# Optimization experiments

Measured on AMD Instinct MI355X. Metric: run time of the kernel, lower is better.

## Reference

```python
import jax, jax.numpy as jnp
import numpy as np

REG = 10.0       # Sinkhorn entropic regularization (module default)
ALPHA = 1e-3     # residual blend coefficient (module default)
N_ITER = 200     # fixed Sinkhorn iterations (POT default numItermax=1000 w/ early stop)


def _sinkhorn(cost):
    """Standard (non-log) Sinkhorn as in POT's ot.sinkhorn. cost: (n, m)."""
    n, m = cost.shape
    a = jnp.full((n,), 1.0 / n, cost.dtype)
    b = jnp.full((m,), 1.0 / m, cost.dtype)
    K = jnp.exp(-cost / REG)                     # (n, m)
    u0 = jnp.full((n,), 1.0 / n, cost.dtype)
    v0 = jnp.full((m,), 1.0 / m, cost.dtype)

    def step(carry, _):
        u, v = carry
        v = b / (K.T @ u)
        u = a / (K @ v)
        return (u, v), None

    (u, v), _ = jax.lax.scan(step, (u0, v0), None, length=N_ITER)
    return (u[:, None] * K) * v[None, :]         # transport plan (n, m)


def setup_inputs() -> dict:
    key = jax.random.key(0)
    k1, k2 = jax.random.split(key)
    sc = jax.random.normal(k1, (4096, 256), dtype=jnp.float32)
    h_spot = jax.random.normal(k2, (4, 256, 48, 48), dtype=jnp.float32)
    return {"sc": sc, "h_spot": h_spot}


def reference(sc, h_spot):
    B, C, H, W = h_spot.shape
    sc_sub = sc[:, :C]                                  # (n_cells, C)
    Y = h_spot.reshape(B, C, H * W).transpose(0, 2, 1)  # (B, HW, C)

    # torch version detaches (numpy round-trip) before the OT solve
    X = jax.lax.stop_gradient(sc_sub)
    Y_sg = jax.lax.stop_gradient(Y)

    # squared Euclidean cost: ot.dist(X, Y, 'euclidean')**2
    x2 = jnp.sum(X * X, axis=-1)                        # (n_cells,)
    y2 = jnp.sum(Y_sg * Y_sg, axis=-1)                  # (B, HW)
    cost = x2[None, :, None] + y2[:, None, :] - 2.0 * jnp.einsum('nc,bmc->bnm', X, Y_sg)
    cost = jnp.maximum(cost, 0.0)                       # (B, n_cells, HW)

    P = jax.vmap(_sinkhorn)(cost)                       # (B, n_cells, HW)
    X_space = jnp.einsum('bnm,nc->bmc', P, X)           # (B, HW, C), detached in torch

    # mean over batch of per-batch MSE == overall mean (equal sizes)
    L_ot = jnp.mean((Y - X_space) ** 2)

    ot_feat = X_space.transpose(0, 2, 1).reshape(B, C, H, W)
    h_spot_aligned = h_spot + ALPHA * ot_feat
    return h_spot_aligned, L_ot, ot_feat
```

## Files before the change

### kernel.cpp

```cpp
#include <hip/hip_runtime.h>
#include <hip/hip_fp16.h>

#define NN 4096
#define NM 2304
#define NC 256
#define OUT_ELEMS 2359296
#define MAX_IT 10

static constexpr float REG_INV = 0.1f;
static constexpr float A_VAL = 1.0f / 4096.0f;
static constexpr float B_VAL = 1.0f / 2304.0f;
static constexpr float ALPHA_C = 0.001f;
static constexpr float EPS_CONV = 1e-4f;
static constexpr float S_Q = 6144.0f;

typedef __attribute__((ext_vector_type(8))) short bf16x8;
typedef __attribute__((ext_vector_type(4))) float f32x4;
typedef __attribute__((ext_vector_type(2))) float f32x2;

__device__ __forceinline__ float bf2f(unsigned short h) {
  return __uint_as_float(((unsigned int)h) << 16);
}
__device__ __forceinline__ unsigned short f2bf(float f) {
  unsigned int u = __float_as_uint(f);
  unsigned int r = (u + 0x7FFFu + ((u >> 16) & 1u)) >> 16;
  return (unsigned short)r;
}
__device__ __forceinline__ unsigned char f2e5(float x) {
  unsigned short h = __half_as_ushort(__float2half_rn(x));
  return (unsigned char)((h + 0x7Fu + ((h >> 8) & 1u)) >> 8);
}
__device__ __forceinline__ float e52f(unsigned int hs) {
  return __half2float(__ushort_as_half((unsigned short)hs));
}
__device__ __forceinline__ void dec4(unsigned int q, float4& o) {
#if __has_builtin(__builtin_amdgcn_cvt_pk_f32_bf8)
  f32x2 lo = __builtin_amdgcn_cvt_pk_f32_bf8((int)q, false);
  f32x2 hi = __builtin_amdgcn_cvt_pk_f32_bf8((int)q, true);
  o.x = lo[0]; o.y = lo[1]; o.z = hi[0]; o.w = hi[1];
#else
  o.x = e52f((q << 8) & 0xFF00u);
  o.y = e52f(q & 0xFF00u);
  o.z = e52f((q >> 8) & 0xFF00u);
  o.w = e52f((q >> 16) & 0xFF00u);
#endif
}
__device__ __forceinline__ float waveSum(float s) {
#pragma unroll
  for (int off = 32; off > 0; off >>= 1) s += __shfl_xor(s, off);
  return s;
}

__global__ __launch_bounds__(256) void x2_kernel(const float* __restrict__ X,
                                                 float* __restrict__ x2) {
  int wid = threadIdx.x >> 6, lane = threadIdx.x & 63;
  int row = blockIdx.x * 4 + wid;
  float4 v = *(const float4*)(X + (size_t)row * NC + lane * 4);
  float s = v.x * v.x + v.y * v.y + v.z * v.z + v.w * v.w;
  s = waveSum(s);
  if (lane == 0) x2[row] = s;
}

__global__ __launch_bounds__(256) void y2_kernel(const float* __restrict__ H,
                                                 float* __restrict__ y2) {
  const int b = blockIdx.y;
  const int m0 = blockIdx.x * 32;
  const int t = threadIdx.x;
  const int ml = t & 31, cg = t >> 5;
  const float* p = H + ((size_t)b * NC + cg) * NM + m0 + ml;
  float s = 0.f;
#pragma unroll 8
  for (int i = 0; i < 32; ++i) {
    float v = p[(size_t)i * 8 * NM];
    s += v * v;
  }
  __shared__ float red[8][33];
  red[cg][ml] = s;
  __syncthreads();
  if (t < 32) {
    float tot = 0.f;
#pragma unroll
    for (int g = 0; g < 8; ++g) tot += red[g][t];
    y2[b * NM + m0 + t] = tot;
  }
}

__global__ __launch_bounds__(256) void prep_xbf(const float* __restrict__ X,
                                                unsigned short* __restrict__ Xbf) {
  size_t i = blockIdx.x * 256 + threadIdx.x;
  float4 xv = *(const float4*)(X + i * 4);
  ushort4 o = {f2bf(xv.x), f2bf(xv.y), f2bf(xv.z), f2bf(xv.w)};
  *(ushort4*)(Xbf + i * 4) = o;
}

__global__ __launch_bounds__(256) void prep_ht(const float* __restrict__ H,
                                               unsigned short* __restrict__ HT) {
  __shared__ unsigned short tile[32][34];
  const int b = blockIdx.z;
  const int mt = blockIdx.x * 32, ct = blockIdx.y * 32;
  const int t = threadIdx.x;
#pragma unroll
  for (int p = 0; p < 4; ++p) {
    int c = ct + p * 8 + (t >> 5);
    tile[t & 31][p * 8 + (t >> 5)] = f2bf(H[((size_t)b * NC + c) * NM + mt + (t & 31)]);
  }
  __syncthreads();
#pragma unroll
  for (int p = 0; p < 4; ++p) {
    int mloc = p * 8 + (t >> 5);
    HT[((size_t)b * NM + mt + mloc) * NC + ct + (t & 31)] = tile[mloc][t & 31];
  }
}

__global__ __launch_bounds__(256) void umax_kernel(const float* __restrict__ uF,
                                                   float* __restrict__ umax) {
  const int b = blockIdx.x, t = threadIdx.x, l = t & 63, wv = t >> 6;
  float mx = 0.f;
  for (int i = t; i < NN; i += 256) mx = fmaxf(mx, uF[b * NN + i]);
#pragma unroll
  for (int off = 32; off > 0; off >>= 1) mx = fmaxf(mx, __shfl_xor(mx, off));
  __shared__ float wm[4];
  if (l == 0) wm[wv] = mx;
  __syncthreads();
  if (t == 0) umax[b] = fmaxf(fmaxf(wm[0], wm[1]), fmaxf(wm[2], wm[3]));
}

__global__ __launch_bounds__(256) void prep_xqu(const float* __restrict__ X,
                                                const float* __restrict__ uF,
                                                const float* __restrict__ umax,
                                                unsigned char* __restrict__ XquT) {
  __shared__ unsigned char tile[32][36];
  const int b = blockIdx.z;
  const int nt = blockIdx.x * 32, ct = blockIdx.y * 32;
  const int t = threadIdx.x;
  const float s = S_Q / umax[b];
#pragma unroll
  for (int p = 0; p < 4; ++p) {
    int nloc = p * 8 + (t >> 5);
    float uu = s * uF[b * NN + nt + nloc];
    tile[nloc][t & 31] = f2e5(uu * X[(size_t)(nt + nloc) * NC + ct + (t & 31)]);
  }
  __syncthreads();
  int cl = t >> 3, seg = t & 7;
  uchar4 o = {tile[seg * 4 + 0][cl], tile[seg * 4 + 1][cl],
              tile[seg * 4 + 2][cl], tile[seg * 4 + 3][cl]};
  *(uchar4*)(XquT + ((size_t)b * NC + ct + cl) * NN + nt + seg * 4) = o;
}

__global__ __launch_bounds__(256) void init_kernel(float* __restrict__ usum0,
                                                   float* __restrict__ u0,
                                                   int* __restrict__ nc) {
  int gid = blockIdx.x * 256 + threadIdx.x;
  usum0[gid] = 1.0f;
  u0[gid] = A_VAL;
  if (gid < 8) nc[gid] = 1;
}

__global__ __launch_bounds__(256) void cost_k_mfma(
    const unsigned short* __restrict__ Xbf, const unsigned short* __restrict__ HT,
    const float* __restrict__ x2, const float* __restrict__ y2,
    unsigned short* __restrict__ KT) {
  __shared__ __align__(16) unsigned short smem[128 * 88];
  const int b = blockIdx.z;
  const int n0 = blockIdx.x * 128, m0 = blockIdx.y * 128;
  const int t = threadIdx.x, l = t & 63, w = t >> 6;
  const int wn = (w >> 1) * 64, wm = (w & 1) * 64;
  const int fr = l & 15, fq = l >> 4;
  f32x4 zero = {0.f, 0.f, 0.f, 0.f};
  f32x4 acc[4][4];
#pragma unroll
  for (int i = 0; i < 4; ++i)
#pragma unroll
    for (int j = 0; j < 4; ++j) acc[i][j] = zero;

  for (int c0 = 0; c0 < NC; c0 += 32) {
#pragma unroll
    for (int i = 0; i < 2; ++i) {
      int idx = t + i * 256;
      int row = idx >> 2, ck = idx & 3;
      float4 av = *(const float4*)(Xbf + (size_t)(n0 + row) * NC + c0 + ck * 8);
      *(float4*)(&smem[row * 44 + ck * 8]) = av;
      float4 bv = *(const float4*)(HT + ((size_t)b * NM + m0 + row) * NC + c0 + ck * 8);
      *(float4*)(&smem[5632 + row * 44 + ck * 8]) = bv;
    }
    __syncthreads();
    bf16x8 a[4], bb[4];
#pragma unroll
    for (int f = 0; f < 4; ++f) {
      a[f] = *(const bf16x8*)(&smem[(wn + f * 16 + fr) * 44 + fq * 8]);
      bb[f] = *(const bf16x8*)(&smem[5632 + (wm + f * 16 + fr) * 44 + fq * 8]);
    }
#pragma unroll
    for (int i = 0; i < 4; ++i)
#pragma unroll
      for (int j = 0; j < 4; ++j)
        acc[i][j] = __builtin_amdgcn_mfma_f32_16x16x32_bf16(a[i], bb[j], acc[i][j], 0, 0, 0);
    __syncthreads();
  }
  float x2a[4][4];
#pragma unroll
  for (int fi = 0; fi < 4; ++fi) {
    float4 xv = *(const float4*)(x2 + n0 + wn + fi * 16 + fq * 4);
    x2a[fi][0] = xv.x; x2a[fi][1] = xv.y; x2a[fi][2] = xv.z; x2a[fi][3] = xv.w;
  }
  float y2a[4];
#pragma unroll
  for (int fj = 0; fj < 4; ++fj) y2a[fj] = y2[b * NM + m0 + wm + fj * 16 + fr];
  unsigned short kb[4][4][4];
#pragma unroll
  for (int fi = 0; fi < 4; ++fi)
#pragma unroll
    for (int fj = 0; fj < 4; ++fj)
#pragma unroll
      for (int r = 0; r < 4; ++r) {
        float cost = fmaxf(x2a[fi][r] + y2a[fj] - 2.0f * acc[fi][fj][r], 0.0f);
        kb[fi][fj][r] = f2bf(__expf(-cost * REG_INV));
      }
#pragma unroll
  for (int h = 0; h < 2; ++h) {
    __syncthreads();
    if ((w & 1) == h) {
#pragma unroll
      for (int fj = 0; fj < 4; ++fj) {
        int rr = fj * 16 + fr;
#pragma unroll
        for (int fi = 0; fi < 4; ++fi) {
          int cc = wn + fi * 16 + fq * 4;
          ushort4 kt4 = {kb[fi][fj][0], kb[fi][fj][1], kb[fi][fj][2], kb[fi][fj][3]};
          *(ushort4*)&smem[rr * 136 + (cc ^ ((rr & 7) << 3))] = kt4;
        }
      }
    }
    __syncthreads();
#pragma unroll
    for (int p = 0; p < 4; ++p) {
      int row = p * 16 + (t >> 4), co = (t & 15) * 8;
      *(float4*)(KT + ((size_t)b * NM + m0 + h * 64 + row) * NN + n0 + co) =
          *(const float4*)&smem[row * 136 + (co ^ ((row & 7) << 3))];
    }
  }
}

__global__ __launch_bounds__(256) void requant_kernel(
    const unsigned short* __restrict__ KT, unsigned char* __restrict__ K8T) {
  const int row = blockIdx.x;
  const int t = threadIdx.x, l = t & 63, wv = t >> 6;
  const unsigned short* src = KT + (size_t)row * NN + t * 16;
  float4 a0 = *(const float4*)(src);
  float4 a1 = *(const float4*)(src + 8);
  const unsigned short* s0 = (const unsigned short*)&a0;
  const unsigned short* s1 = (const unsigned short*)&a1;
  float mx = 0.f;
#pragma unroll
  for (int j = 0; j < 8; ++j)
    mx = fmaxf(mx, fmaxf(bf2f(s0[j]), bf2f(s1[j])));
#pragma unroll
  for (int off = 32; off > 0; off >>= 1) mx = fmaxf(mx, __shfl_xor(mx, off));
  __shared__ float wmx[4];
  if (l == 0) wmx[wv] = mx;
  __syncthreads();
  mx = fmaxf(fmaxf(wmx[0], wmx[1]), fmaxf(wmx[2], wmx[3]));
  float c = fminf(32768.0f / mx, 1e38f);
  unsigned int o[4] = {0, 0, 0, 0};
#pragma unroll
  for (int j = 0; j < 8; ++j) {
    o[j >> 2] |= (unsigned int)f2e5(bf2f(s0[j]) * c) << ((j & 3) * 8);
    o[2 + (j >> 2)] |= (unsigned int)f2e5(bf2f(s1[j]) * c) << ((j & 3) * 8);
  }
  uint4 ov = {o[0], o[1], o[2], o[3]};
  *(uint4*)(K8T + (size_t)row * NN + t * 16) = ov;
}

__global__ __launch_bounds__(256) void vrow_kernel(
    const unsigned char* __restrict__ K8T, const float* __restrict__ usumR,
    float* __restrict__ usumZ, const float* __restrict__ uR,
    float* __restrict__ uW, float* __restrict__ uF, float* __restrict__ vB,
    const int* __restrict__ ncG, int* __restrict__ ncS, int force) {
  const int b = blockIdx.y, bx = blockIdx.x;
  const int t = threadIdx.x, l = t & 63, wv = t >> 6;
  if (bx == 0 && t == 0) ncS[b] = 0;
  if (ncG[b] == 0) return;
  __shared__ __align__(16) float uS[NN];
  int flag = force;
#pragma unroll
  for (int jj = 0; jj < 16; ++jj) {
    int i = jj * 256 + t;
    float us = usumR[b * NN + i];
    float uo = uR[b * NN + i];
    float ut = A_VAL / us;
    float r = ut / uo;
    float un = uo * r * sqrtf(sqrtf(r));
    uS[i] = un;
    if (bx == 0) {
      uW[b * NN + i] = un;
      uF[b * NN + i] = un;
      if (fabsf(ut - uo) > EPS_CONV * uo) flag = 1;
    }
    if (bx == 1) usumZ[b * NN + i] = 0.f;
  }
  __syncthreads();
  if (bx == 0 && flag) ncS[b] = 1;
  const unsigned char* KTb = K8T + (size_t)(b * NM + bx * 12) * NN;
#pragma unroll 1
  for (int rr = 0; rr < 3; ++rr) {
    int row = wv * 3 + rr;
    const unsigned int* Kp = (const unsigned int*)(KTb + (size_t)row * NN);
    float s = 0.f;
#pragma unroll
    for (int p = 0; p < 16; ++p) {
      unsigned int q = Kp[l + 64 * p];
      float4 d;
      dec4(q, d);
      float4 uu = ((const float4*)uS)[l + 64 * p];
      s += d.x * uu.x + d.y * uu.y + d.z * uu.z + d.w * uu.w;
    }
    s = waveSum(s);
    if (l == 0) vB[b * NM + bx * 12 + row] = B_VAL / s;
  }
}

__global__ __launch_bounds__(256) void ucol_kernel(
    const unsigned char* __restrict__ K8T, const float* __restrict__ vB,
    float* __restrict__ usumA, const int* __restrict__ ncG) {
  const int b = blockIdx.z;
  if (ncG[b] == 0) return;
  const int nch = blockIdx.x;
  const int mch = blockIdx.y;
  const int t = threadIdx.x, l = t & 63, wv = t >> 6;
  __shared__ float vS[288];
  __shared__ __align__(16) float red[4][64][4];
  for (int i = t; i < 288; i += 256) vS[i] = vB[b * NM + mch * 288 + i];
  __syncthreads();
  const unsigned char* Kp =
      K8T + (size_t)(b * NM + mch * 288) * NN + nch * 256 + l * 4;
  float4 acc = {0.f, 0.f, 0.f, 0.f};
#pragma unroll 8
  for (int i = 0; i < 72; ++i) {
    int m = i * 4 + wv;
    unsigned int q = *(const unsigned int*)(Kp + (size_t)m * NN);
    float4 d;
    dec4(q, d);
    float vv = vS[m];
    acc.x += d.x * vv;
    acc.y += d.y * vv;
    acc.z += d.z * vv;
    acc.w += d.w * vv;
  }
  *(float4*)red[wv][l] = acc;
  __syncthreads();
  if (wv == 0) {
    float4 a0 = *(float4*)red[0][l];
    float4 a1 = *(float4*)red[1][l];
    float4 a2 = *(float4*)red[2][l];
    float4 a3 = *(float4*)red[3][l];
    float* dst = usumA + (size_t)b * NN + nch * 256 + l * 4;
    atomicAdd(dst + 0, a0.x + a1.x + a2.x + a3.x);
    atomicAdd(dst + 1, a0.y + a1.y + a2.y + a3.y);
    atomicAdd(dst + 2, a0.z + a1.z + a2.z + a3.z);
    atomicAdd(dst + 3, a0.w + a1.w + a2.w + a3.w);
  }
}

__global__ __launch_bounds__(256) void xspace_bf8(
    const unsigned char* __restrict__ XquT, const unsigned char* __restrict__ K8T,
    const float* __restrict__ vB, const float* __restrict__ umax,
    float* __restrict__ XT0, float* __restrict__ XT1) {
  __shared__ __align__(16) unsigned char As[64][80];
  __shared__ __align__(16) unsigned char Bs[64][80];
  const int b = blockIdx.z & 3, kh = blockIdx.z >> 2;
  const int c0 = blockIdx.x * 64, m0 = blockIdx.y * 64;
  const int t = threadIdx.x, l = t & 63, w = t >> 6;
  const int wc = (w >> 1) * 32, wm = (w & 1) * 32;
  const int fr = l & 15, fq = l >> 4;
  f32x4 zero = {0.f, 0.f, 0.f, 0.f};
  f32x4 acc[2][2];
#pragma unroll
  for (int i = 0; i < 2; ++i)
#pragma unroll
    for (int j = 0; j < 2; ++j) acc[i][j] = zero;

  const int srow = t >> 2, sseg = t & 3;
  const int kbeg = kh * 2048;
  for (int k0 = kbeg; k0 < kbeg + 2048; k0 += 64) {
    *(uint4*)&As[srow][sseg * 16] = *(const uint4*)(
        XquT + ((size_t)b * NC + c0 + srow) * NN + k0 + sseg * 16);
    *(uint4*)&Bs[srow][sseg * 16] = *(const uint4*)(
        K8T + ((size_t)b * NM + m0 + srow) * NN + k0 + sseg * 16);
    __syncthreads();
    long long a[2][2], bb[2][2];
#pragma unroll
    for (int f = 0; f < 2; ++f)
#pragma unroll
      for (int ks = 0; ks < 2; ++ks) {
        a[f][ks] = *(const long long*)&As[wc + f * 16 + fr][ks * 32 + fq * 8];
        bb[f][ks] = *(const long long*)&Bs[wm + f * 16 + fr][ks * 32 + fq * 8];
      }
#pragma unroll
    for (int ks = 0; ks < 2; ++ks)
#pragma unroll
      for (int i = 0; i < 2; ++i)
#pragma unroll
        for (int j = 0; j < 2; ++j)
          acc[i][j] = __builtin_amdgcn_mfma_f32_16x16x32_bf8_bf8(
              a[i][ks], bb[j][ks], acc[i][j], 0, 0, 0);
    __syncthreads();
  }
  const float sb = umax[b] * (1.0f / S_Q);
  float* XTo = kh ? XT1 : XT0;
#pragma unroll
  for (int fj = 0; fj < 2; ++fj) {
    int m = m0 + wm + fj * 16 + fr;
    float vm = vB[(size_t)b * NM + m] * sb;
#pragma unroll
    for (int fi = 0; fi < 2; ++fi) {
      int cb = c0 + wc + fi * 16 + fq * 4;
#pragma unroll
      for (int r = 0; r < 4; ++r)
        XTo[((size_t)b * NC + cb + r) * NM + m] = vm * acc[fi][fj][r];
    }
  }
}

__global__ __launch_bounds__(256) void finalize_kernel(
    const float* __restrict__ H, const float* __restrict__ XT0,
    const float* __restrict__ XT1, float* __restrict__ out_aligned,
    float* __restrict__ out_feat, float* __restrict__ partials) {
  const int t = threadIdx.x;
  float s = 0.f;
  for (int i = blockIdx.x * 256 + t; i < OUT_ELEMS / 4; i += 1024 * 256) {
    float4 h = *(const float4*)(H + (size_t)i * 4);
    float4 xa = *(const float4*)(XT0 + (size_t)i * 4);
    float4 xb = *(const float4*)(XT1 + (size_t)i * 4);
    float4 x;
    x.x = xa.x + xb.x;
    x.y = xa.y + xb.y;
    x.z = xa.z + xb.z;
    x.w = xa.w + xb.w;
    float4 o;
    o.x = h.x + ALPHA_C * x.x;
    o.y = h.y + ALPHA_C * x.y;
    o.z = h.z + ALPHA_C * x.z;
    o.w = h.w + ALPHA_C * x.w;
    *(float4*)(out_aligned + (size_t)i * 4) = o;
    out_feat[(size_t)i * 4 + 0] = x.x;
    out_feat[(size_t)i * 4 + 1] = x.y;
    out_feat[(size_t)i * 4 + 2] = x.z;
    out_feat[(size_t)i * 4 + 3] = x.w;
    float dx = h.x - x.x, dy = h.y - x.y, dz = h.z - x.z, dw = h.w - x.w;
    s += dx * dx + dy * dy + dz * dz + dw * dw;
  }
  s = waveSum(s);
  __shared__ float ws_[4];
  if ((t & 63) == 0) ws_[t >> 6] = s;
  __syncthreads();
  if (t == 0) partials[blockIdx.x] = ws_[0] + ws_[1] + ws_[2] + ws_[3];
}

__global__ __launch_bounds__(256) void lot_kernel(
    const float* __restrict__ partials, float* __restrict__ out_lot) {
  float s = 0.f;
  for (int i = threadIdx.x; i < 1024; i += 256) s += partials[i];
  s = waveSum(s);
  __shared__ float ws_[4];
  if ((threadIdx.x & 63) == 0) ws_[threadIdx.x >> 6] = s;
  __syncthreads();
  if (threadIdx.x == 0)
    out_lot[0] = (ws_[0] + ws_[1] + ws_[2] + ws_[3]) / (float)OUT_ELEMS;
}

extern "C" void kernel_launch(void* const* d_in, const int* in_sizes, int n_in,
                              void* d_out, int out_size, void* d_ws,
                              size_t ws_size, hipStream_t stream) {
  const float* X = (const float*)d_in[0];
  const float* H = (const float*)d_in[1];
  float* out = (float*)d_out;
  char* ws = (char*)d_ws;

  unsigned short* KT = (unsigned short*)(ws);
  unsigned char* XquT = (unsigned char*)(ws);
  unsigned char* K8T = (unsigned char*)(ws + 75497472);
  float* XT0 = (float*)(ws + 113246208);
  unsigned short* Xbf = (unsigned short*)(ws + 113246208);
  unsigned short* HT = (unsigned short*)(ws + 113246208 + 2097152);
  float* usum = (float*)(ws + 122683392);
  float* u = (float*)(ws + 122814464);
  float* uF = (float*)(ws + 122945536);
  float* vB = (float*)(ws + 123011072);
  float* x2 = (float*)(ws + 123047936);
  float* y2 = (float*)(ws + 123064320);
  int* nc = (int*)(ws + 123101184);
  float* partials = (float*)(ws + 123101216);
  float* umax = (float*)(ws + 123105312);
  float* XT1 = (float*)(ws + 134217728);
  if (ws_size < (size_t)143654912) return;

  x2_kernel<<<1024, 256, 0, stream>>>(X, x2);
  y2_kernel<<<dim3(72, 4), 256, 0, stream>>>(H, y2);
  prep_xbf<<<1024, 256, 0, stream>>>(X, Xbf);
  prep_ht<<<dim3(72, 8, 4), 256, 0, stream>>>(H, HT);
  cost_k_mfma<<<dim3(32, 18, 4), 256, 0, stream>>>(Xbf, HT, x2, y2, KT);
  requant_kernel<<<9216, 256, 0, stream>>>(KT, K8T);
  init_kernel<<<64, 256, 0, stream>>>(usum, u, nc);
  for (int it = 0; it < MAX_IT; ++it) {
    const int p = it & 1, q = 1 - p;
    vrow_kernel<<<dim3(192, 4), 256, 0, stream>>>(
        K8T, usum + (size_t)p * 4 * NN, usum + (size_t)q * 4 * NN,
        u + (size_t)p * 4 * NN, u + (size_t)q * 4 * NN, uF, vB,
        nc + q * 4, nc + p * 4, it == 0 ? 1 : 0);
    ucol_kernel<<<dim3(16, 8, 4), 256, 0, stream>>>(
        K8T, vB, usum + (size_t)q * 4 * NN, nc + q * 4);
  }
  umax_kernel<<<4, 256, 0, stream>>>(uF, umax);
  prep_xqu<<<dim3(128, 8, 4), 256, 0, stream>>>(X, uF, umax, XquT);
  xspace_bf8<<<dim3(4, 36, 8), 256, 0, stream>>>(XquT, K8T, vB, umax, XT0, XT1);
  finalize_kernel<<<1024, 256, 0, stream>>>(H, XT0, XT1, out,
                                            out + OUT_ELEMS + 1, partials);
  lot_kernel<<<1, 256, 0, stream>>>(partials, out + OUT_ELEMS);
}
```

Baseline: 384.8 us.

## Fuse preprocessing kernels and widen Sinkhorn matvec loads to 16 bytes

Merges the x2 and bf16-X conversion into one kernel, folds the y2 row-norm computation into the H transpose kernel using atomics, and combines the init kernels. The Sinkhorn vrow and ucol kernels now load 16 bytes of fp8 K per lane instead of 4. vrow permutes its shared u layout to match the new load pattern, and ucol is retiled to a 4x32 grid with every thread issuing atomics. The aim is fewer launches and wider global loads in the bandwidth-bound iteration loop. In exchange, more atomics go to usum and y2 summation order becomes nondeterministic.

```diff
diff --git a/kernel.cpp b/kernel.cpp
--- a/kernel.cpp
+++ b/kernel.cpp
@@ -51,64 +51,59 @@
   return s;
 }
 
-__global__ __launch_bounds__(256) void x2_kernel(const float* __restrict__ X,
-                                                 float* __restrict__ x2) {
+__global__ __launch_bounds__(256) void init0_kernel(float* __restrict__ usum0,
+                                                    float* __restrict__ u0,
+                                                    float* __restrict__ y2,
+                                                    int* __restrict__ nc) {
+  int gid = blockIdx.x * 256 + threadIdx.x;
+  usum0[gid] = 1.0f;
+  u0[gid] = A_VAL;
+  if (gid < 4 * NM) y2[gid] = 0.f;
+  if (gid < 8) nc[gid] = 1;
+}
+
+__global__ __launch_bounds__(256) void xprep_kernel(const float* __restrict__ X,
+                                                    float* __restrict__ x2,
+                                                    unsigned short* __restrict__ Xbf) {
   int wid = threadIdx.x >> 6, lane = threadIdx.x & 63;
   int row = blockIdx.x * 4 + wid;
   float4 v = *(const float4*)(X + (size_t)row * NC + lane * 4);
+  ushort4 o = {f2bf(v.x), f2bf(v.y), f2bf(v.z), f2bf(v.w)};
+  *(ushort4*)(Xbf + (size_t)row * NC + lane * 4) = o;
   float s = v.x * v.x + v.y * v.y + v.z * v.z + v.w * v.w;
   s = waveSum(s);
   if (lane == 0) x2[row] = s;
 }
 
-__global__ __launch_bounds__(256) void y2_kernel(const float* __restrict__ H,
-                                                 float* __restrict__ y2) {
-  const int b = blockIdx.y;
-  const int m0 = blockIdx.x * 32;
-  const int t = threadIdx.x;
-  const int ml = t & 31, cg = t >> 5;
-  const float* p = H + ((size_t)b * NC + cg) * NM + m0 + ml;
-  float s = 0.f;
-#pragma unroll 8
-  for (int i = 0; i < 32; ++i) {
-    float v = p[(size_t)i * 8 * NM];
-    s += v * v;
-  }
-  __shared__ float red[8][33];
-  red[cg][ml] = s;
-  __syncthreads();
-  if (t < 32) {
-    float tot = 0.f;
-#pragma unroll
-    for (int g = 0; g < 8; ++g) tot += red[g][t];
-    y2[b * NM + m0 + t] = tot;
-  }
-}
-
-__global__ __launch_bounds__(256) void prep_xbf(const float* __restrict__ X,
-                                                unsigned short* __restrict__ Xbf) {
-  size_t i = blockIdx.x * 256 + threadIdx.x;
-  float4 xv = *(const float4*)(X + i * 4);
-  ushort4 o = {f2bf(xv.x), f2bf(xv.y), f2bf(xv.z), f2bf(xv.w)};
-  *(ushort4*)(Xbf + i * 4) = o;
-}
-
-__global__ __launch_bounds__(256) void prep_ht(const float* __restrict__ H,
-                                               unsigned short* __restrict__ HT) {
+__global__ __launch_bounds__(256) void ht_y2_kernel(const float* __restrict__ H,
+                                                    unsigned short* __restrict__ HT,
+                                                    float* __restrict__ y2) {
   __shared__ unsigned short tile[32][34];
+  __shared__ float redY[8][33];
   const int b = blockIdx.z;
   const int mt = blockIdx.x * 32, ct = blockIdx.y * 32;
   const int t = threadIdx.x;
+  float ss = 0.f;
 #pragma unroll
   for (int p = 0; p < 4; ++p) {
     int c = ct + p * 8 + (t >> 5);
-    tile[t & 31][p * 8 + (t >> 5)] = f2bf(H[((size_t)b * NC + c) * NM + mt + (t & 31)]);
+    float hv = H[((size_t)b * NC + c) * NM + mt + (t & 31)];
+    tile[t & 31][p * 8 + (t >> 5)] = f2bf(hv);
+    ss += hv * hv;
   }
   __syncthreads();
 #pragma unroll
   for (int p = 0; p < 4; ++p) {
     int mloc = p * 8 + (t >> 5);
     HT[((size_t)b * NM + mt + mloc) * NC + ct + (t & 31)] = tile[mloc][t & 31];
+  }
+  redY[t >> 5][t & 31] = ss;
+  __syncthreads();
+  if (t < 32) {
+    float tot = 0.f;
+#pragma unroll
+    for (int g = 0; g < 8; ++g) tot += redY[g][t];
+    atomicAdd(&y2[b * NM + mt + t], tot);
   }
 }
 
@@ -145,15 +140,6 @@
   uchar4 o = {tile[seg * 4 + 0][cl], tile[seg * 4 + 1][cl],
               tile[seg * 4 + 2][cl], tile[seg * 4 + 3][cl]};
   *(uchar4*)(XquT + ((size_t)b * NC + ct + cl) * NN + nt + seg * 4) = o;
-}
-
-__global__ __launch_bounds__(256) void init_kernel(float* __restrict__ usum0,
-                                                   float* __restrict__ u0,
-                                                   int* __restrict__ nc) {
-  int gid = blockIdx.x * 256 + threadIdx.x;
-  usum0[gid] = 1.0f;
-  u0[gid] = A_VAL;
-  if (gid < 8) nc[gid] = 1;
 }
 
 __global__ __launch_bounds__(256) void cost_k_mfma(
@@ -290,7 +276,9 @@
     float ut = A_VAL / us;
     float r = ut / uo;
     float un = uo * r * sqrtf(sqrtf(r));
-    uS[i] = un;
+    int fidx = (jj >> 2) * 1024 + ((t >> 2) & 3) * 256 +
+               ((jj & 3) * 16 + (t >> 4)) * 4 + (t & 3);
+    uS[fidx] = un;
     if (bx == 0) {
       uW[b * NN + i] = un;
       uF[b * NN + i] = un;
@@ -300,18 +288,28 @@
   }
   __syncthreads();
   if (bx == 0 && flag) ncS[b] = 1;
+  const float4* uS4 = (const float4*)uS;
   const unsigned char* KTb = K8T + (size_t)(b * NM + bx * 12) * NN;
 #pragma unroll 1
   for (int rr = 0; rr < 3; ++rr) {
     int row = wv * 3 + rr;
-    const unsigned int* Kp = (const unsigned int*)(KTb + (size_t)row * NN);
+    const uint4* Kp4 = (const uint4*)(KTb + (size_t)row * NN);
     float s = 0.f;
 #pragma unroll
-    for (int p = 0; p < 16; ++p) {
-      unsigned int q = Kp[l + 64 * p];
-      float4 d;
-      dec4(q, d);
-      float4 uu = ((const float4*)uS)[l + 64 * p];
+    for (int p = 0; p < 4; ++p) {
+      uint4 q4 = Kp4[p * 64 + l];
+      float4 d, uu;
+      dec4(q4.x, d);
+      uu = uS4[p * 256 + 0 * 64 + l];
+      s += d.x * uu.x + d.y * uu.y + d.z * uu.z + d.w * uu.w;
+      dec4(q4.y, d);
+      uu = uS4[p * 256 + 1 * 64 + l];
+      s += d.x * uu.x + d.y * uu.y + d.z * uu.z + d.w * uu.w;
+      dec4(q4.z, d);
+      uu = uS4[p * 256 + 2 * 64 + l];
+      s += d.x * uu.x + d.y * uu.y + d.z * uu.z + d.w * uu.w;
+      dec4(q4.w, d);
+      uu = uS4[p * 256 + 3 * 64 + l];
       s += d.x * uu.x + d.y * uu.y + d.z * uu.z + d.w * uu.w;
     }
     s = waveSum(s);
@@ -327,38 +325,44 @@
   const int nch = blockIdx.x;
   const int mch = blockIdx.y;
   const int t = threadIdx.x, l = t & 63, wv = t >> 6;
-  __shared__ float vS[288];
-  __shared__ __align__(16) float red[4][64][4];
-  for (int i = t; i < 288; i += 256) vS[i] = vB[b * NM + mch * 288 + i];
+  __shared__ float vS[72];
+  __shared__ __align__(16) float4 red4[1024];
+  if (t < 72) vS[t] = vB[b * NM + mch * 72 + t];
   __syncthreads();
   const unsigned char* Kp =
-      K8T + (size_t)(b * NM + mch * 288) * NN + nch * 256 + l * 4;
-  float4 acc = {0.f, 0.f, 0.f, 0.f};
-#pragma unroll 8
-  for (int i = 0; i < 72; ++i) {
+      K8T + (size_t)(b * NM + mch * 72) * NN + nch * 1024 + l * 16;
+  float4 p0 = {0.f, 0.f, 0.f, 0.f}, p1 = p0, p2 = p0, p3 = p0;
+#pragma unroll 3
+  for (int i = 0; i < 18; ++i) {
     int m = i * 4 + wv;
-    unsigned int q = *(const unsigned int*)(Kp + (size_t)m * NN);
+    uint4 q4 = *(const uint4*)(Kp + (size_t)m * NN);
+    float vv = vS[m];
     float4 d;
-    dec4(q, d);
-    float vv = vS[m];
-    acc.x += d.x * vv;
-    acc.y += d.y * vv;
-    acc.z += d.z * vv;
-    acc.w += d.w * vv;
-  }
-  *(float4*)red[wv][l] = acc;
-  __syncthreads();
-  if (wv == 0) {
-    float4 a0 = *(float4*)red[0][l];
-    float4 a1 = *(float4*)red[1][l];
-    float4 a2 = *(float4*)red[2][l];
-    float4 a3 = *(float4*)red[3][l];
-    float* dst = usumA + (size_t)b * NN + nch * 256 + l * 4;
-    atomicAdd(dst + 0, a0.x + a1.x + a2.x + a3.x);
-    atomicAdd(dst + 1, a0.y + a1.y + a2.y + a3.y);
-    atomicAdd(dst + 2, a0.z + a1.z + a2.z + a3.z);
-    atomicAdd(dst + 3, a0.w + a1.w + a2.w + a3.w);
-  }
+    dec4(q4.x, d);
+    p0.x += d.x * vv; p0.y += d.y * vv; p0.z += d.z * vv; p0.w += d.w * vv;
+    dec4(q4.y, d);
+    p1.x += d.x * vv; p1.y += d.y * vv; p1.z += d.z * vv; p1.w += d.w * vv;
+    dec4(q4.z, d);
+    p2.x += d.x * vv; p2.y += d.y * vv; p2.z += d.z * vv; p2.w += d.w * vv;
+    dec4(q4.w, d);
+    p3.x += d.x * vv; p3.y += d.y * vv; p3.z += d.z * vv; p3.w += d.w * vv;
+  }
+  red4[wv * 256 + 0 * 64 + l] = p0;
+  red4[wv * 256 + 1 * 64 + l] = p1;
+  red4[wv * 256 + 2 * 64 + l] = p2;
+  red4[wv * 256 + 3 * 64 + l] = p3;
+  __syncthreads();
+  float4 s0 = red4[t], s1 = red4[256 + t], s2 = red4[512 + t], s3 = red4[768 + t];
+  float4 sum;
+  sum.x = s0.x + s1.x + s2.x + s3.x;
+  sum.y = s0.y + s1.y + s2.y + s3.y;
+  sum.z = s0.z + s1.z + s2.z + s3.z;
+  sum.w = s0.w + s1.w + s2.w + s3.w;
+  float* dst = usumA + (size_t)b * NN + nch * 1024 + 16 * (t & 63) + 4 * (t >> 6);
+  atomicAdd(dst + 0, sum.x);
+  atomicAdd(dst + 1, sum.y);
+  atomicAdd(dst + 2, sum.z);
+  atomicAdd(dst + 3, sum.w);
 }
 
 __global__ __launch_bounds__(256) void xspace_bf8(
@@ -494,20 +498,18 @@
   float* XT1 = (float*)(ws + 134217728);
   if (ws_size < (size_t)143654912) return;
 
-  x2_kernel<<<1024, 256, 0, stream>>>(X, x2);
-  y2_kernel<<<dim3(72, 4), 256, 0, stream>>>(H, y2);
-  prep_xbf<<<1024, 256, 0, stream>>>(X, Xbf);
-  prep_ht<<<dim3(72, 8, 4), 256, 0, stream>>>(H, HT);
+  init0_kernel<<<64, 256, 0, stream>>>(usum, u, y2, nc);
+  xprep_kernel<<<1024, 256, 0, stream>>>(X, x2, Xbf);
+  ht_y2_kernel<<<dim3(72, 8, 4), 256, 0, stream>>>(H, HT, y2);
   cost_k_mfma<<<dim3(32, 18, 4), 256, 0, stream>>>(Xbf, HT, x2, y2, KT);
   requant_kernel<<<9216, 256, 0, stream>>>(KT, K8T);
-  init_kernel<<<64, 256, 0, stream>>>(usum, u, nc);
   for (int it = 0; it < MAX_IT; ++it) {
     const int p = it & 1, q = 1 - p;
     vrow_kernel<<<dim3(192, 4), 256, 0, stream>>>(
         K8T, usum + (size_t)p * 4 * NN, usum + (size_t)q * 4 * NN,
         u + (size_t)p * 4 * NN, u + (size_t)q * 4 * NN, uF, vB,
         nc + q * 4, nc + p * 4, it == 0 ? 1 : 0);
-    ucol_kernel<<<dim3(16, 8, 4), 256, 0, stream>>>(
+    ucol_kernel<<<dim3(4, 32, 4), 256, 0, stream>>>(
         K8T, vB, usum + (size_t)q * 4 * NN, nc + q * 4);
   }
   umax_kernel<<<4, 256, 0, stream>>>(uF, umax);
```

After: 637.8 us. 1.66x slower.
